# Kernel optimization log

Hardware: AMD Instinct MI355X
Metric: run time of the kernel (lower is better)

Reference implementation:

```python
import jax, jax.numpy as jnp
import numpy as np
from jax import lax

SIGMA = 10.0


def _maxpool3(x):
    # x: (1, N, D, H, W), kernel 3, stride 1, VALID
    return lax.reduce_window(x, -jnp.inf, lax.max,
                             (1, 1, 3, 3, 3), (1, 1, 1, 1, 1), 'VALID')


def _avgpool3(x):
    s = lax.reduce_window(x, 0.0, lax.add,
                          (1, 1, 3, 3, 3), (1, 1, 1, 1, 1), 'VALID')
    return s / 27.0


def _smooth(x):
    # ReplicationPad3d(3) -> MaxPool3d(3,1) -> AvgPool3d(3,1) x2 ; keeps spatial size
    x = jnp.pad(x, ((0, 0), (0, 0), (3, 3), (3, 3), (3, 3)), mode='edge')
    return _avgpool3(_avgpool3(_maxpool3(x)))


def setup_inputs() -> dict:
    key = jax.random.key(0)
    k1, k2, k3 = jax.random.split(key, 3)
    N, K, L = 10000, 8, 13
    cost = jax.random.normal(k1, (N, 1, L, L, L), dtype=jnp.float32)
    knn = jax.random.randint(k2, (N, K), 0, N)
    dist_nn = jax.random.uniform(k3, (N, K), dtype=jnp.float32) * 20.0
    alpha = jnp.array([1.0, 0.1, 1.0, 1.0, 0.1, 1.0], dtype=jnp.float32)
    return {"cost": cost, "knn": knn, "dist_nn": dist_nn, "alpha": alpha}


def reference(cost, knn, dist_nn, alpha):
    N = cost.shape[0]
    L = cost.shape[2]
    cost = alpha[1] + alpha[0] * cost                       # (N,1,L,L,L)
    w = jnp.exp(-dist_nn / (2.0 * SIGMA ** 2))              # (N,K)
    norm = w.sum(axis=1)                                    # (N,)
    cost = cost.reshape(1, N, L, L, L)

    cost_approx = _smooth(cost)                             # (1,N,L,L,L)
    # gather K neighbors and do distance-weighted mean
    nbr = cost_approx[:, knn]                               # (1,N,K,L,L,L)
    cost_approx = jnp.einsum('ankxyz,nk->anxyz', nbr, w)
    cost_approx = cost_approx / norm[None, :, None, None, None]

    cost = alpha[4] + alpha[2] * cost + alpha[3] * cost_approx
    cost = _smooth(cost)
    nbr = cost[:, knn]                                      # (1,N,K,L,L,L)
    cost = jnp.einsum('ankxyz,nk->anxyz', nbr, w)
    cost = cost / norm[None, :, None, None, None]
    return alpha[5] * cost.reshape(1, N, -1)
```

## Files before the change

### kernel.cpp

```cpp
#include <hip/hip_runtime.h>
#include <math.h>

#define L3 2197
#define SP 2200
#define NV (SP / 8)
#define NT 256

#define ASZ 3760
#define BSZ 4916

typedef unsigned int u32;

__device__ __forceinline__ u32 pack2bf(float a, float b) {
    u32 ua = __float_as_uint(a);
    u32 ub = __float_as_uint(b);
    ua = (ua + 0x7fffu + ((ua >> 16) & 1u)) >> 16;
    ub = (ub + 0x7fffu + ((ub >> 16) & 1u)) & 0xffff0000u;
    return ua | ub;
}

__device__ __forceinline__ void unpack8(uint4 v, float* f) {
    f[0] = __uint_as_float(v.x << 16);
    f[1] = __uint_as_float(v.x & 0xffff0000u);
    f[2] = __uint_as_float(v.y << 16);
    f[3] = __uint_as_float(v.y & 0xffff0000u);
    f[4] = __uint_as_float(v.z << 16);
    f[5] = __uint_as_float(v.z & 0xffff0000u);
    f[6] = __uint_as_float(v.w << 16);
    f[7] = __uint_as_float(v.w & 0xffff0000u);
}

__device__ __forceinline__ uint4 pack8(const float* f) {
    uint4 v;
    v.x = pack2bf(f[0], f[1]);
    v.y = pack2bf(f[2], f[3]);
    v.z = pack2bf(f[4], f[5]);
    v.w = pack2bf(f[6], f[7]);
    return v;
}

__device__ __forceinline__ void maxpool_row(const float* x, float* o) {
    float p[12];
#pragma unroll
    for (int i = 0; i < 12; ++i) p[i] = fmaxf(x[i], x[i + 1]);
    o[0] = x[0];
    o[1] = x[0];
    o[2] = p[0];
#pragma unroll
    for (int j = 3; j <= 13; ++j) o[j] = fmaxf(p[j - 3], x[j - 1]);
    o[14] = p[11];
    o[15] = x[12];
    o[16] = x[12];
}

__device__ __forceinline__ void tri_row(const float* y, float* o, float scale) {
#pragma unroll
    for (int c = 0; c < 13; ++c) {
        float s = fmaf(2.0f, y[c + 1], y[c]);
        s = fmaf(3.0f, y[c + 2], s);
        s = fmaf(2.0f, y[c + 3], s);
        o[c] = (s + y[c + 4]) * scale;
    }
}

__device__ void smooth_inplace(float* A, float* B, int tid) {
    __syncthreads();
    if (tid < 169) {
        float x[13], o[17];
        const float* src = A + tid * 13;
#pragma unroll
        for (int i = 0; i < 13; ++i) x[i] = src[i];
        maxpool_row(x, o);
        float* dst = B + tid * 17;
#pragma unroll
        for (int i = 0; i < 17; ++i) dst[i] = o[i];
    }
    __syncthreads();
    if (tid < 221) {
        int a = tid / 17, c = tid % 17;
        float x[13], o[17];
        const float* src = B + a * 221 + c;
#pragma unroll
        for (int i = 0; i < 13; ++i) x[i] = src[i * 17];
        maxpool_row(x, o);
        float* dst = A + a * 289 + c;
#pragma unroll
        for (int i = 0; i < 17; ++i) dst[i * 17] = o[i];
    }
    __syncthreads();
    for (int p = tid; p < 289; p += NT) {
        float x[13], o[17];
        const float* src = A + p;
#pragma unroll
        for (int i = 0; i < 13; ++i) x[i] = src[i * 289];
        maxpool_row(x, o);
        float* dst = B + p;
#pragma unroll
        for (int i = 0; i < 17; ++i) dst[i * 289] = o[i];
    }
    __syncthreads();
    for (int p = tid; p < 289; p += NT) {
        float y[17], o[13];
        const float* src = B + p * 17;
#pragma unroll
        for (int i = 0; i < 17; ++i) y[i] = src[i];
        tri_row(y, o, 1.0f);
        float* dst = A + p * 13;
#pragma unroll
        for (int i = 0; i < 13; ++i) dst[i] = o[i];
    }
    __syncthreads();
    if (tid < 221) {
        int a = tid / 13, c = tid % 13;
        float y[17], o[13];
        const float* src = A + a * 221 + c;
#pragma unroll
        for (int i = 0; i < 17; ++i) y[i] = src[i * 13];
        tri_row(y, o, 1.0f);
        float* dst = B + a * 169 + c;
#pragma unroll
        for (int i = 0; i < 13; ++i) dst[i * 13] = o[i];
    }
    __syncthreads();
    if (tid < 169) {
        float y[17], o[13];
        const float* src = B + tid;
#pragma unroll
        for (int i = 0; i < 17; ++i) y[i] = src[i * 169];
        tri_row(y, o, 1.0f / 729.0f);
        float* dst = A + tid;
#pragma unroll
        for (int i = 0; i < 13; ++i) dst[i * 169] = o[i];
    }
    __syncthreads();
}

__global__ __launch_bounds__(NT) void k_smooth1(
        const float* __restrict__ cost, const float* __restrict__ alpha,
        uint4* __restrict__ tmp1, uint4* __restrict__ preA) {
    __shared__ alignas(16) float A[ASZ];
    __shared__ alignas(16) float B[BSZ];
    const int n = blockIdx.x;
    const int tid = threadIdx.x;
    const float a0 = alpha[0], a1 = alpha[1], a2 = alpha[2], a4 = alpha[4];
    const float* src = cost + (size_t)n * L3;
    for (int i = tid; i < L3; i += NT) A[i] = fmaf(a0, src[i], a1);
    if (tid < SP - L3) A[L3 + tid] = 0.0f;
    __syncthreads();
    uint4* pre = preA + (size_t)n * NV;
    for (int i = tid; i < NV; i += NT) {
        float f[8];
#pragma unroll
        for (int j = 0; j < 8; ++j) f[j] = fmaf(a2, A[8 * i + j], a4);
        pre[i] = pack8(f);
    }
    smooth_inplace(A, B, tid);
    uint4* dst = tmp1 + (size_t)n * NV;
    for (int i = tid; i < NV; i += NT) {
        float f[8];
#pragma unroll
        for (int j = 0; j < 8; ++j) f[j] = A[8 * i + j];
        dst[i] = pack8(f);
    }
}

__global__ __launch_bounds__(NT) void k_mid(
        const int* __restrict__ knn, const float* __restrict__ dist,
        const float* __restrict__ alpha, const uint4* __restrict__ tmp1,
        const uint4* __restrict__ preA, uint4* __restrict__ tmp2, int K) {
    __shared__ alignas(16) float A[ASZ];
    __shared__ alignas(16) float B[BSZ];
    __shared__ float s_w[8];
    const int n = blockIdx.x;
    const int tid = threadIdx.x;
    if (tid < K) s_w[tid] = expf(-dist[n * K + tid] * (1.0f / 200.0f));
    __syncthreads();
    float norm = 0.0f;
    for (int k = 0; k < K; ++k) norm += s_w[k];
    const float sc = alpha[3] / norm;

    const uint4* ptr[8];
    float wk[8];
    for (int k = 0; k < K; ++k) {
        ptr[k] = tmp1 + (size_t)knn[n * K + k] * NV;
        wk[k] = s_w[k];
    }
    const uint4* pre = preA + (size_t)n * NV;
    for (int i = tid; i < NV; i += NT) {
        float f[8], acc[8], g[8];
        unpack8(pre[i], f);
#pragma unroll
        for (int j = 0; j < 8; ++j) acc[j] = 0.0f;
#pragma unroll 8
        for (int k = 0; k < K; ++k) {
            unpack8(ptr[k][i], g);
#pragma unroll
            for (int j = 0; j < 8; ++j) acc[j] = fmaf(wk[k], g[j], acc[j]);
        }
#pragma unroll
        for (int j = 0; j < 8; ++j) A[8 * i + j] = fmaf(sc, acc[j], f[j]);
    }
    smooth_inplace(A, B, tid);
    uint4* dst = tmp2 + (size_t)n * NV;
    for (int i = tid; i < NV; i += NT) {
        float f[8];
#pragma unroll
        for (int j = 0; j < 8; ++j) f[j] = A[8 * i + j];
        dst[i] = pack8(f);
    }
}

__global__ __launch_bounds__(NT) void k_out(
        const int* __restrict__ knn, const float* __restrict__ dist,
        const float* __restrict__ alpha, const uint4* __restrict__ tmp2,
        float* __restrict__ out, int K) {
    __shared__ float s_w[8];
    const int n = blockIdx.x;
    const int tid = threadIdx.x;
    if (tid < K) s_w[tid] = expf(-dist[n * K + tid] * (1.0f / 200.0f));
    __syncthreads();
    float norm = 0.0f;
    for (int k = 0; k < K; ++k) norm += s_w[k];
    const float sc = alpha[5] / norm;

    const uint4* ptr[8];
    float wk[8];
    for (int k = 0; k < K; ++k) {
        ptr[k] = tmp2 + (size_t)knn[n * K + k] * NV;
        wk[k] = s_w[k];
    }
    float* dst = out + (size_t)n * L3;
    for (int i = tid; i < NV; i += NT) {
        float acc[8], g[8];
#pragma unroll
        for (int j = 0; j < 8; ++j) acc[j] = 0.0f;
#pragma unroll 8
        for (int k = 0; k < K; ++k) {
            unpack8(ptr[k][i], g);
#pragma unroll
            for (int j = 0; j < 8; ++j) acc[j] = fmaf(wk[k], g[j], acc[j]);
        }
        int base = 8 * i;
#pragma unroll
        for (int j = 0; j < 8; ++j)
            if (base + j < L3) dst[base + j] = sc * acc[j];
    }
}

extern "C" void kernel_launch(void* const* d_in, const int* in_sizes, int n_in,
                              void* d_out, int out_size, void* d_ws, size_t ws_size,
                              hipStream_t stream) {
    const float* cost  = (const float*)d_in[0];
    const int*   knn   = (const int*)d_in[1];
    const float* dist  = (const float*)d_in[2];
    const float* alpha = (const float*)d_in[3];
    float* out = (float*)d_out;

    const int N = in_sizes[0] / L3;
    int K = in_sizes[1] / N;
    if (K > 8) K = 8;

    uint4* tmp1 = (uint4*)d_ws;
    uint4* tmp2 = tmp1 + (size_t)N * NV;
    uint4* preA = tmp2 + (size_t)N * NV;

    k_smooth1<<<N, NT, 0, stream>>>(cost, alpha, tmp1, preA);
    k_mid<<<N, NT, 0, stream>>>(knn, dist, alpha, tmp1, preA, tmp2, K);
    k_out<<<N, NT, 0, stream>>>(knn, dist, alpha, tmp2, out, K);
}
```

Before: 359.8 us.

## Use single in-place shared buffer for smoothing with 320-thread blocks

Replaces the two ping-pong shared buffers (A, B) in the smoothing stages with one 4913-float buffer. Each pass now reads into registers, synchronises, then writes back in place. The smoothing kernels move to 320 threads so the 289-wide passes run in one iteration. This roughly halves LDS per block so more blocks can be resident per CU, at the cost of an extra barrier per pass and idle threads in the narrower passes.

```diff
diff --git a/kernel.cpp b/kernel.cpp
--- a/kernel.cpp
+++ b/kernel.cpp
@@ -4,10 +4,10 @@
 #define L3 2197
 #define SP 2200
 #define NV (SP / 8)
-#define NT 256
-
-#define ASZ 3760
-#define BSZ 4916
+#define NTS 320
+#define NTO 256
+
+#define SSZ 4913
 
 typedef unsigned int u32;
 
@@ -63,113 +63,136 @@
     }
 }
 
-__device__ void smooth_inplace(float* A, float* B, int tid) {
-    __syncthreads();
-    if (tid < 169) {
+__device__ void smooth_single(float* S, int tid) {
+    __syncthreads();
+    {
+        const bool act = tid < 169;
         float x[13], o[17];
-        const float* src = A + tid * 13;
-#pragma unroll
-        for (int i = 0; i < 13; ++i) x[i] = src[i];
-        maxpool_row(x, o);
-        float* dst = B + tid * 17;
-#pragma unroll
-        for (int i = 0; i < 17; ++i) dst[i] = o[i];
-    }
-    __syncthreads();
-    if (tid < 221) {
-        int a = tid / 17, c = tid % 17;
+        if (act) {
+            const float* src = S + tid * 13;
+#pragma unroll
+            for (int i = 0; i < 13; ++i) x[i] = src[i];
+            maxpool_row(x, o);
+        }
+        __syncthreads();
+        if (act) {
+            float* d = S + tid * 17;
+#pragma unroll
+            for (int i = 0; i < 17; ++i) d[i] = o[i];
+        }
+        __syncthreads();
+    }
+    {
+        const bool act = tid < 221;
+        const int a = tid / 17, c = tid % 17;
         float x[13], o[17];
-        const float* src = B + a * 221 + c;
-#pragma unroll
-        for (int i = 0; i < 13; ++i) x[i] = src[i * 17];
-        maxpool_row(x, o);
-        float* dst = A + a * 289 + c;
-#pragma unroll
-        for (int i = 0; i < 17; ++i) dst[i * 17] = o[i];
-    }
-    __syncthreads();
-    for (int p = tid; p < 289; p += NT) {
+        if (act) {
+            const float* src = S + a * 221 + c;
+#pragma unroll
+            for (int i = 0; i < 13; ++i) x[i] = src[i * 17];
+            maxpool_row(x, o);
+        }
+        __syncthreads();
+        if (act) {
+            float* d = S + a * 289 + c;
+#pragma unroll
+            for (int i = 0; i < 17; ++i) d[i * 17] = o[i];
+        }
+        __syncthreads();
+    }
+    if (tid < 289) {
         float x[13], o[17];
-        const float* src = A + p;
+        const float* src = S + tid;
 #pragma unroll
         for (int i = 0; i < 13; ++i) x[i] = src[i * 289];
         maxpool_row(x, o);
-        float* dst = B + p;
-#pragma unroll
-        for (int i = 0; i < 17; ++i) dst[i * 289] = o[i];
-    }
-    __syncthreads();
-    for (int p = tid; p < 289; p += NT) {
+        float* d = S + tid;
+#pragma unroll
+        for (int i = 0; i < 17; ++i) d[i * 289] = o[i];
+    }
+    __syncthreads();
+    {
+        const bool act = tid < 289;
         float y[17], o[13];
-        const float* src = B + p * 17;
-#pragma unroll
-        for (int i = 0; i < 17; ++i) y[i] = src[i];
-        tri_row(y, o, 1.0f);
-        float* dst = A + p * 13;
-#pragma unroll
-        for (int i = 0; i < 13; ++i) dst[i] = o[i];
-    }
-    __syncthreads();
-    if (tid < 221) {
-        int a = tid / 13, c = tid % 13;
+        if (act) {
+            const float* src = S + tid * 17;
+#pragma unroll
+            for (int i = 0; i < 17; ++i) y[i] = src[i];
+            tri_row(y, o, 1.0f);
+        }
+        __syncthreads();
+        if (act) {
+            float* d = S + tid * 13;
+#pragma unroll
+            for (int i = 0; i < 13; ++i) d[i] = o[i];
+        }
+        __syncthreads();
+    }
+    {
+        const bool act = tid < 221;
+        const int a = tid / 13, c = tid % 13;
         float y[17], o[13];
-        const float* src = A + a * 221 + c;
-#pragma unroll
-        for (int i = 0; i < 17; ++i) y[i] = src[i * 13];
-        tri_row(y, o, 1.0f);
-        float* dst = B + a * 169 + c;
-#pragma unroll
-        for (int i = 0; i < 13; ++i) dst[i * 13] = o[i];
-    }
-    __syncthreads();
+        if (act) {
+            const float* src = S + a * 221 + c;
+#pragma unroll
+            for (int i = 0; i < 17; ++i) y[i] = src[i * 13];
+            tri_row(y, o, 1.0f);
+        }
+        __syncthreads();
+        if (act) {
+            float* d = S + a * 169 + c;
+#pragma unroll
+            for (int i = 0; i < 13; ++i) d[i * 13] = o[i];
+        }
+        __syncthreads();
+    }
     if (tid < 169) {
         float y[17], o[13];
-        const float* src = B + tid;
+        const float* src = S + tid;
 #pragma unroll
         for (int i = 0; i < 17; ++i) y[i] = src[i * 169];
         tri_row(y, o, 1.0f / 729.0f);
-        float* dst = A + tid;
-#pragma unroll
-        for (int i = 0; i < 13; ++i) dst[i * 169] = o[i];
-    }
-    __syncthreads();
-}
-
-__global__ __launch_bounds__(NT) void k_smooth1(
+        float* d = S + tid;
+#pragma unroll
+        for (int i = 0; i < 13; ++i) d[i * 169] = o[i];
+    }
+    __syncthreads();
+}
+
+__global__ __launch_bounds__(NTS) void k_smooth1(
         const float* __restrict__ cost, const float* __restrict__ alpha,
         uint4* __restrict__ tmp1, uint4* __restrict__ preA) {
-    __shared__ alignas(16) float A[ASZ];
-    __shared__ alignas(16) float B[BSZ];
+    __shared__ alignas(16) float S[SSZ];
     const int n = blockIdx.x;
     const int tid = threadIdx.x;
     const float a0 = alpha[0], a1 = alpha[1], a2 = alpha[2], a4 = alpha[4];
     const float* src = cost + (size_t)n * L3;
-    for (int i = tid; i < L3; i += NT) A[i] = fmaf(a0, src[i], a1);
-    if (tid < SP - L3) A[L3 + tid] = 0.0f;
+    for (int i = tid; i < L3; i += NTS) S[i] = fmaf(a0, src[i], a1);
+    if (tid < SP - L3) S[L3 + tid] = 0.0f;
     __syncthreads();
     uint4* pre = preA + (size_t)n * NV;
-    for (int i = tid; i < NV; i += NT) {
+    if (tid < NV) {
         float f[8];
 #pragma unroll
-        for (int j = 0; j < 8; ++j) f[j] = fmaf(a2, A[8 * i + j], a4);
-        pre[i] = pack8(f);
-    }
-    smooth_inplace(A, B, tid);
+        for (int j = 0; j < 8; ++j) f[j] = fmaf(a2, S[8 * tid + j], a4);
+        pre[tid] = pack8(f);
+    }
+    smooth_single(S, tid);
     uint4* dst = tmp1 + (size_t)n * NV;
-    for (int i = tid; i < NV; i += NT) {
+    if (tid < NV) {
         float f[8];
-#pragma unroll
-        for (int j = 0; j < 8; ++j) f[j] = A[8 * i + j];
-        dst[i] = pack8(f);
-    }
-}
-
-__global__ __launch_bounds__(NT) void k_mid(
+        const int base = 8 * tid;
+#pragma unroll
+        for (int j = 0; j < 8; ++j) f[j] = (base + j < L3) ? S[base + j] : 0.0f;
+        dst[tid] = pack8(f);
+    }
+}
+
+__global__ __launch_bounds__(NTS) void k_mid(
         const int* __restrict__ knn, const float* __restrict__ dist,
         const float* __restrict__ alpha, const uint4* __restrict__ tmp1,
         const uint4* __restrict__ preA, uint4* __restrict__ tmp2, int K) {
-    __shared__ alignas(16) float A[ASZ];
-    __shared__ alignas(16) float B[BSZ];
+    __shared__ alignas(16) float S[SSZ];
     __shared__ float s_w[8];
     const int n = blockIdx.x;
     const int tid = threadIdx.x;
@@ -186,31 +209,32 @@
         wk[k] = s_w[k];
     }
     const uint4* pre = preA + (size_t)n * NV;
-    for (int i = tid; i < NV; i += NT) {
+    if (tid < NV) {
         float f[8], acc[8], g[8];
-        unpack8(pre[i], f);
+        unpack8(pre[tid], f);
 #pragma unroll
         for (int j = 0; j < 8; ++j) acc[j] = 0.0f;
 #pragma unroll 8
         for (int k = 0; k < K; ++k) {
-            unpack8(ptr[k][i], g);
+            unpack8(ptr[k][tid], g);
 #pragma unroll
             for (int j = 0; j < 8; ++j) acc[j] = fmaf(wk[k], g[j], acc[j]);
         }
 #pragma unroll
-        for (int j = 0; j < 8; ++j) A[8 * i + j] = fmaf(sc, acc[j], f[j]);
-    }
-    smooth_inplace(A, B, tid);
+        for (int j = 0; j < 8; ++j) S[8 * tid + j] = fmaf(sc, acc[j], f[j]);
+    }
+    smooth_single(S, tid);
     uint4* dst = tmp2 + (size_t)n * NV;
-    for (int i = tid; i < NV; i += NT) {
+    if (tid < NV) {
         float f[8];
-#pragma unroll
-        for (int j = 0; j < 8; ++j) f[j] = A[8 * i + j];
-        dst[i] = pack8(f);
-    }
-}
-
-__global__ __launch_bounds__(NT) void k_out(
+        const int base = 8 * tid;
+#pragma unroll
+        for (int j = 0; j < 8; ++j) f[j] = (base + j < L3) ? S[base + j] : 0.0f;
+        dst[tid] = pack8(f);
+    }
+}
+
+__global__ __launch_bounds__(NTO) void k_out(
         const int* __restrict__ knn, const float* __restrict__ dist,
         const float* __restrict__ alpha, const uint4* __restrict__ tmp2,
         float* __restrict__ out, int K) {
@@ -230,7 +254,7 @@
         wk[k] = s_w[k];
     }
     float* dst = out + (size_t)n * L3;
-    for (int i = tid; i < NV; i += NT) {
+    for (int i = tid; i < NV; i += NTO) {
         float acc[8], g[8];
 #pragma unroll
         for (int j = 0; j < 8; ++j) acc[j] = 0.0f;
@@ -240,7 +264,7 @@
 #pragma unroll
             for (int j = 0; j < 8; ++j) acc[j] = fmaf(wk[k], g[j], acc[j]);
         }
-        int base = 8 * i;
+        const int base = 8 * i;
 #pragma unroll
         for (int j = 0; j < 8; ++j)
             if (base + j < L3) dst[base + j] = sc * acc[j];
@@ -264,7 +288,7 @@
     uint4* tmp2 = tmp1 + (size_t)N * NV;
     uint4* preA = tmp2 + (size_t)N * NV;
 
-    k_smooth1<<<N, NT, 0, stream>>>(cost, alpha, tmp1, preA);
-    k_mid<<<N, NT, 0, stream>>>(knn, dist, alpha, tmp1, preA, tmp2, K);
-    k_out<<<N, NT, 0, stream>>>(knn, dist, alpha, tmp2, out, K);
-}
+    k_smooth1<<<N, NTS, 0, stream>>>(cost, alpha, tmp1, preA);
+    k_mid<<<N, NTS, 0, stream>>>(knn, dist, alpha, tmp1, preA, tmp2, K);
+    k_out<<<N, NTO, 0, stream>>>(knn, dist, alpha, tmp2, out, K);
+}
```

Result: faster. 336.4 us (-6.5%).

## Use single padded in-place LDS volume and row-padded bf16 intermediate layout

Applied to the files above, without the earlier changes.

Replaces the two ping-pong shared buffers with a single padded in-place volume (row pitch 20, plane pitch 344). It fuses the third maxpool pass with the first avgpool pass and uses float4 LDS accesses for contiguous rows. The intermediate bf16 tensors are stored as 338 uint4 chunks per voxel grid, two per row with padding, so the packed layout matches the row structure. This grows intermediate traffic from 275 to 338 chunks per item, and block sizes rise to 320 and 384 threads. The aim is fewer barriers, a smaller shared footprint for more occupancy, and fewer LDS bank conflicts, paid for with about 23% more gather bytes.

```diff
diff --git a/kernel.cpp b/kernel.cpp
--- a/kernel.cpp
+++ b/kernel.cpp
@@ -2,12 +2,13 @@
 #include <math.h>
 
 #define L3 2197
-#define SP 2200
-#define NV (SP / 8)
-#define NT 256
-
-#define ASZ 3760
-#define BSZ 4916
+#define NROW 169
+#define NC 338
+#define RP 20
+#define AP 344
+#define RSZ 5844
+#define NTS 320
+#define NTO 384
 
 typedef unsigned int u32;
 
@@ -63,113 +64,130 @@
     }
 }
 
-__device__ void smooth_inplace(float* A, float* B, int tid) {
-    __syncthreads();
-    if (tid < 169) {
+__device__ void smooth_R(float* R, int tid) {
+    if (tid < NROW) {
+        int a = tid / 13, b = tid - 13 * a;
+        float* row = R + a * AP + b * RP;
         float x[13], o[17];
-        const float* src = A + tid * 13;
-#pragma unroll
-        for (int i = 0; i < 13; ++i) x[i] = src[i];
+        float4 v0 = *(const float4*)row;
+        float4 v1 = *(const float4*)(row + 4);
+        float4 v2 = *(const float4*)(row + 8);
+        x[0] = v0.x; x[1] = v0.y; x[2] = v0.z; x[3] = v0.w;
+        x[4] = v1.x; x[5] = v1.y; x[6] = v1.z; x[7] = v1.w;
+        x[8] = v2.x; x[9] = v2.y; x[10] = v2.z; x[11] = v2.w;
+        x[12] = row[12];
         maxpool_row(x, o);
-        float* dst = B + tid * 17;
-#pragma unroll
-        for (int i = 0; i < 17; ++i) dst[i] = o[i];
+        *(float4*)row       = make_float4(o[0], o[1], o[2], o[3]);
+        *(float4*)(row + 4) = make_float4(o[4], o[5], o[6], o[7]);
+        *(float4*)(row + 8) = make_float4(o[8], o[9], o[10], o[11]);
+        *(float4*)(row + 12) = make_float4(o[12], o[13], o[14], o[15]);
+        row[16] = o[16];
     }
     __syncthreads();
     if (tid < 221) {
-        int a = tid / 17, c = tid % 17;
+        int a = tid / 17, c = tid - 17 * a;
+        float* base = R + a * AP + c;
         float x[13], o[17];
-        const float* src = B + a * 221 + c;
-#pragma unroll
-        for (int i = 0; i < 13; ++i) x[i] = src[i * 17];
+#pragma unroll
+        for (int i = 0; i < 13; ++i) x[i] = base[i * RP];
         maxpool_row(x, o);
-        float* dst = A + a * 289 + c;
-#pragma unroll
-        for (int i = 0; i < 17; ++i) dst[i * 17] = o[i];
-    }
-    __syncthreads();
-    for (int p = tid; p < 289; p += NT) {
-        float x[13], o[17];
-        const float* src = A + p;
-#pragma unroll
-        for (int i = 0; i < 13; ++i) x[i] = src[i * 289];
-        maxpool_row(x, o);
-        float* dst = B + p;
-#pragma unroll
-        for (int i = 0; i < 17; ++i) dst[i * 289] = o[i];
-    }
-    __syncthreads();
-    for (int p = tid; p < 289; p += NT) {
+#pragma unroll
+        for (int i = 0; i < 17; ++i) base[i * RP] = o[i];
+    }
+    __syncthreads();
+    if (tid < 289) {
+        int b = tid / 17, c = tid - 17 * b;
+        float* base = R + b * RP + c;
+        float x[13], m[17], o[13];
+#pragma unroll
+        for (int i = 0; i < 13; ++i) x[i] = base[i * AP];
+        maxpool_row(x, m);
+        tri_row(m, o, 1.0f);
+#pragma unroll
+        for (int i = 0; i < 13; ++i) base[i * AP] = o[i];
+    }
+    __syncthreads();
+    if (tid < 221) {
+        int a = tid / 17, c = tid - 17 * a;
+        float* base = R + a * AP + c;
         float y[17], o[13];
-        const float* src = B + p * 17;
-#pragma unroll
-        for (int i = 0; i < 17; ++i) y[i] = src[i];
+#pragma unroll
+        for (int i = 0; i < 17; ++i) y[i] = base[i * RP];
         tri_row(y, o, 1.0f);
-        float* dst = A + p * 13;
-#pragma unroll
-        for (int i = 0; i < 13; ++i) dst[i] = o[i];
-    }
-    __syncthreads();
-    if (tid < 221) {
-        int a = tid / 13, c = tid % 13;
+#pragma unroll
+        for (int i = 0; i < 13; ++i) base[i * RP] = o[i];
+    }
+    __syncthreads();
+    if (tid < NROW) {
+        int a = tid / 13, b = tid - 13 * a;
+        float* row = R + a * AP + b * RP;
         float y[17], o[13];
-        const float* src = A + a * 221 + c;
-#pragma unroll
-        for (int i = 0; i < 17; ++i) y[i] = src[i * 13];
-        tri_row(y, o, 1.0f);
-        float* dst = B + a * 169 + c;
-#pragma unroll
-        for (int i = 0; i < 13; ++i) dst[i * 13] = o[i];
-    }
-    __syncthreads();
-    if (tid < 169) {
-        float y[17], o[13];
-        const float* src = B + tid;
-#pragma unroll
-        for (int i = 0; i < 17; ++i) y[i] = src[i * 169];
+        float4 v0 = *(const float4*)row;
+        float4 v1 = *(const float4*)(row + 4);
+        float4 v2 = *(const float4*)(row + 8);
+        float4 v3 = *(const float4*)(row + 12);
+        y[0] = v0.x; y[1] = v0.y; y[2] = v0.z; y[3] = v0.w;
+        y[4] = v1.x; y[5] = v1.y; y[6] = v1.z; y[7] = v1.w;
+        y[8] = v2.x; y[9] = v2.y; y[10] = v2.z; y[11] = v2.w;
+        y[12] = v3.x; y[13] = v3.y; y[14] = v3.z; y[15] = v3.w;
+        y[16] = row[16];
         tri_row(y, o, 1.0f / 729.0f);
-        float* dst = A + tid;
-#pragma unroll
-        for (int i = 0; i < 13; ++i) dst[i * 169] = o[i];
-    }
-    __syncthreads();
-}
-
-__global__ __launch_bounds__(NT) void k_smooth1(
+        *(float4*)row       = make_float4(o[0], o[1], o[2], o[3]);
+        *(float4*)(row + 4) = make_float4(o[4], o[5], o[6], o[7]);
+        *(float4*)(row + 8) = make_float4(o[8], o[9], o[10], o[11]);
+        row[12] = o[12];
+    }
+    __syncthreads();
+}
+
+__device__ __forceinline__ void pack_rows(const float* R, uint4* dst, int tid, int nt) {
+    for (int j = tid; j < NC; j += nt) {
+        int r = j >> 1, h = j & 1;
+        int a = r / 13, b = r - 13 * a;
+        const float* p = R + a * AP + b * RP + h * 8;
+        float4 u = *(const float4*)p;
+        float4 v = *(const float4*)(p + 4);
+        float f[8] = {u.x, u.y, u.z, u.w, v.x, v.y, v.z, v.w};
+        if (h) { f[5] = 0.0f; f[6] = 0.0f; f[7] = 0.0f; }
+        dst[j] = pack8(f);
+    }
+}
+
+__global__ __launch_bounds__(NTS) void k_smooth1(
         const float* __restrict__ cost, const float* __restrict__ alpha,
         uint4* __restrict__ tmp1, uint4* __restrict__ preA) {
-    __shared__ alignas(16) float A[ASZ];
-    __shared__ alignas(16) float B[BSZ];
+    __shared__ alignas(16) float R[RSZ];
     const int n = blockIdx.x;
     const int tid = threadIdx.x;
     const float a0 = alpha[0], a1 = alpha[1], a2 = alpha[2], a4 = alpha[4];
     const float* src = cost + (size_t)n * L3;
-    for (int i = tid; i < L3; i += NT) A[i] = fmaf(a0, src[i], a1);
-    if (tid < SP - L3) A[L3 + tid] = 0.0f;
-    __syncthreads();
-    uint4* pre = preA + (size_t)n * NV;
-    for (int i = tid; i < NV; i += NT) {
-        float f[8];
-#pragma unroll
-        for (int j = 0; j < 8; ++j) f[j] = fmaf(a2, A[8 * i + j], a4);
-        pre[i] = pack8(f);
-    }
-    smooth_inplace(A, B, tid);
-    uint4* dst = tmp1 + (size_t)n * NV;
-    for (int i = tid; i < NV; i += NT) {
-        float f[8];
-#pragma unroll
-        for (int j = 0; j < 8; ++j) f[j] = A[8 * i + j];
-        dst[i] = pack8(f);
-    }
-}
-
-__global__ __launch_bounds__(NT) void k_mid(
+    uint4* pre = preA + (size_t)n * NC;
+    for (int j = tid; j < NC; j += NTS) {
+        int r = j >> 1, h = j & 1;
+        int a = r / 13, b = r - 13 * a;
+        const int gbase = r * 13 + h * 8;
+        float f[8], g[8];
+#pragma unroll
+        for (int t = 0; t < 8; ++t) {
+            const int c = h * 8 + t;
+            f[t] = (c < 13) ? fmaf(a0, src[gbase + t], a1) : 0.0f;
+            g[t] = (c < 13) ? fmaf(a2, f[t], a4) : 0.0f;
+        }
+        float* p = R + a * AP + b * RP + h * 8;
+        *(float4*)p       = make_float4(f[0], f[1], f[2], f[3]);
+        *(float4*)(p + 4) = make_float4(f[4], f[5], f[6], f[7]);
+        pre[j] = pack8(g);
+    }
+    __syncthreads();
+    smooth_R(R, tid);
+    pack_rows(R, tmp1 + (size_t)n * NC, tid, NTS);
+}
+
+__global__ __launch_bounds__(NTS) void k_mid(
         const int* __restrict__ knn, const float* __restrict__ dist,
         const float* __restrict__ alpha, const uint4* __restrict__ tmp1,
         const uint4* __restrict__ preA, uint4* __restrict__ tmp2, int K) {
-    __shared__ alignas(16) float A[ASZ];
-    __shared__ alignas(16) float B[BSZ];
+    __shared__ alignas(16) float R[RSZ];
     __shared__ float s_w[8];
     const int n = blockIdx.x;
     const int tid = threadIdx.x;
@@ -182,35 +200,35 @@
     const uint4* ptr[8];
     float wk[8];
     for (int k = 0; k < K; ++k) {
-        ptr[k] = tmp1 + (size_t)knn[n * K + k] * NV;
+        ptr[k] = tmp1 + (size_t)knn[n * K + k] * NC;
         wk[k] = s_w[k];
     }
-    const uint4* pre = preA + (size_t)n * NV;
-    for (int i = tid; i < NV; i += NT) {
+    const uint4* pre = preA + (size_t)n * NC;
+    for (int j = tid; j < NC; j += NTS) {
         float f[8], acc[8], g[8];
-        unpack8(pre[i], f);
-#pragma unroll
-        for (int j = 0; j < 8; ++j) acc[j] = 0.0f;
+        unpack8(pre[j], f);
+#pragma unroll
+        for (int t = 0; t < 8; ++t) acc[t] = 0.0f;
 #pragma unroll 8
         for (int k = 0; k < K; ++k) {
-            unpack8(ptr[k][i], g);
-#pragma unroll
-            for (int j = 0; j < 8; ++j) acc[j] = fmaf(wk[k], g[j], acc[j]);
+            unpack8(ptr[k][j], g);
+#pragma unroll
+            for (int t = 0; t < 8; ++t) acc[t] = fmaf(wk[k], g[t], acc[t]);
         }
-#pragma unroll
-        for (int j = 0; j < 8; ++j) A[8 * i + j] = fmaf(sc, acc[j], f[j]);
-    }
-    smooth_inplace(A, B, tid);
-    uint4* dst = tmp2 + (size_t)n * NV;
-    for (int i = tid; i < NV; i += NT) {
-        float f[8];
-#pragma unroll
-        for (int j = 0; j < 8; ++j) f[j] = A[8 * i + j];
-        dst[i] = pack8(f);
-    }
-}
-
-__global__ __launch_bounds__(NT) void k_out(
+        const int r = j >> 1, h = j & 1;
+        const int a = r / 13, b = r - 13 * a;
+        float* p = R + a * AP + b * RP + h * 8;
+        *(float4*)p = make_float4(fmaf(sc, acc[0], f[0]), fmaf(sc, acc[1], f[1]),
+                                  fmaf(sc, acc[2], f[2]), fmaf(sc, acc[3], f[3]));
+        *(float4*)(p + 4) = make_float4(fmaf(sc, acc[4], f[4]), fmaf(sc, acc[5], f[5]),
+                                        fmaf(sc, acc[6], f[6]), fmaf(sc, acc[7], f[7]));
+    }
+    __syncthreads();
+    smooth_R(R, tid);
+    pack_rows(R, tmp2 + (size_t)n * NC, tid, NTS);
+}
+
+__global__ __launch_bounds__(NTO) void k_out(
         const int* __restrict__ knn, const float* __restrict__ dist,
         const float* __restrict__ alpha, const uint4* __restrict__ tmp2,
         float* __restrict__ out, int K) {
@@ -226,24 +244,25 @@
     const uint4* ptr[8];
     float wk[8];
     for (int k = 0; k < K; ++k) {
-        ptr[k] = tmp2 + (size_t)knn[n * K + k] * NV;
+        ptr[k] = tmp2 + (size_t)knn[n * K + k] * NC;
         wk[k] = s_w[k];
     }
     float* dst = out + (size_t)n * L3;
-    for (int i = tid; i < NV; i += NT) {
+    for (int j = tid; j < NC; j += NTO) {
         float acc[8], g[8];
 #pragma unroll
-        for (int j = 0; j < 8; ++j) acc[j] = 0.0f;
+        for (int t = 0; t < 8; ++t) acc[t] = 0.0f;
 #pragma unroll 8
         for (int k = 0; k < K; ++k) {
-            unpack8(ptr[k][i], g);
-#pragma unroll
-            for (int j = 0; j < 8; ++j) acc[j] = fmaf(wk[k], g[j], acc[j]);
+            unpack8(ptr[k][j], g);
+#pragma unroll
+            for (int t = 0; t < 8; ++t) acc[t] = fmaf(wk[k], g[t], acc[t]);
         }
-        int base = 8 * i;
-#pragma unroll
-        for (int j = 0; j < 8; ++j)
-            if (base + j < L3) dst[base + j] = sc * acc[j];
+        const int r = j >> 1, h = j & 1;
+        const int gbase = r * 13 + h * 8;
+#pragma unroll
+        for (int t = 0; t < 8; ++t)
+            if (h * 8 + t < 13) dst[gbase + t] = sc * acc[t];
     }
 }
 
@@ -261,10 +280,10 @@
     if (K > 8) K = 8;
 
     uint4* tmp1 = (uint4*)d_ws;
-    uint4* tmp2 = tmp1 + (size_t)N * NV;
-    uint4* preA = tmp2 + (size_t)N * NV;
-
-    k_smooth1<<<N, NT, 0, stream>>>(cost, alpha, tmp1, preA);
-    k_mid<<<N, NT, 0, stream>>>(knn, dist, alpha, tmp1, preA, tmp2, K);
-    k_out<<<N, NT, 0, stream>>>(knn, dist, alpha, tmp2, out, K);
-}
+    uint4* tmp2 = tmp1 + (size_t)N * NC;
+    uint4* preA = tmp2 + (size_t)N * NC;
+
+    k_smooth1<<<N, NTS, 0, stream>>>(cost, alpha, tmp1, preA);
+    k_mid<<<N, NTS, 0, stream>>>(knn, dist, alpha, tmp1, preA, tmp2, K);
+    k_out<<<N, NTO, 0, stream>>>(knn, dist, alpha, tmp2, out, K);
+}
```

New measurement: 348.0 us. 1.03x faster.
